# Performance work log

Measured on AMD Instinct MI355X. Metric: run time of the kernel, lower is better.

Reference implementation:

```python
import jax, jax.numpy as jnp
import numpy as np

EPS = 1e-8


def quaternion_mul(q, m):
    # Hamilton product q * m over last dim of size 4 (w, x, y, z)
    w1, x1, y1, z1 = q[..., 0], q[..., 1], q[..., 2], q[..., 3]
    w2, x2, y2, z2 = m[..., 0], m[..., 1], m[..., 2], m[..., 3]
    return jnp.stack([
        w1 * w2 - x1 * x2 - y1 * y2 - z1 * z2,
        w1 * x2 + x1 * w2 + y1 * z2 - z1 * y2,
        w1 * y2 - x1 * z2 + y1 * w2 + z1 * x2,
        w1 * z2 + x1 * y2 - y1 * x2 + z1 * w2,
    ], axis=-1)


def quaternion_normalize(q):
    n = jnp.linalg.norm(q, axis=-1, keepdims=True)
    return q / (n + EPS)


def setup_inputs() -> dict:
    key = jax.random.key(0)
    k = jax.random.split(key, 5)
    B, S, D, H = 4, 2048, 1024, 1024
    scale = 0.02
    return {
        "x": jax.random.normal(k[0], (B, S, D), dtype=jnp.float32),
        "W_in": jax.random.normal(k[1], (3 * H, D), dtype=jnp.float32) * scale,
        "b_in": jax.random.normal(k[2], (3 * H,), dtype=jnp.float32) * scale,
        "W_out": jax.random.normal(k[3], (D, 4 * H), dtype=jnp.float32) * scale,
        "b_out": jax.random.normal(k[4], (D,), dtype=jnp.float32) * scale,
    }


def reference(x, W_in, b_in, W_out, b_out):
    B, S, D = x.shape
    H = W_in.shape[0] // 3
    # input projection -> rotation parameters v in R^3 per hidden channel
    v = (jnp.einsum('bsd,ed->bse', x, W_in) + b_in).reshape(B, S, H, 3)
    # SU(2) exponential map: v -> unit quaternion
    theta = jnp.linalg.norm(v, axis=-1, keepdims=True)          # (B,S,H,1)
    axis = v / (theta + EPS)
    q_inputs = jnp.concatenate([jnp.cos(theta), jnp.sin(theta) * axis], axis=-1)  # (B,S,H,4)

    # initial identity quaternion state (B,H,4)
    m0 = jnp.zeros((B, H, 4), dtype=x.dtype).at[..., 0].set(1.0)

    def step(m, q_t):
        m_new = quaternion_normalize(quaternion_mul(q_t, m))
        return m_new, m_new

    q_seq = jnp.transpose(q_inputs, (1, 0, 2, 3))               # (S,B,H,4)
    m_final, ms = jax.lax.scan(step, m0, q_seq)                 # ms: (S,B,H,4)

    states = jnp.transpose(ms, (1, 0, 2, 3)).reshape(B, S, 4 * H)
    full_output = jnp.einsum('bsf,df->bsd', states, W_out) + b_out
    return full_output, m_final
```

## Files before the change

### kernel.cpp

```cpp
#include <hip/hip_runtime.h>
#include <hip/hip_bf16.h>
#include <stdint.h>

#define EPSF 1e-8f

typedef __attribute__((ext_vector_type(8))) short short8;
typedef __attribute__((ext_vector_type(8))) _Float16 half8;
typedef __attribute__((ext_vector_type(4))) float floatx4;

__device__ __forceinline__ unsigned short f2h(float f) {
    _Float16 h = (_Float16)f;
    return __builtin_bit_cast(unsigned short, h);
}
__device__ __forceinline__ float h2f(unsigned short u) {
    return (float)__builtin_bit_cast(_Float16, u);
}


__global__ void prep_kernel(const float4* __restrict__ x4, ushort4* __restrict__ x16,
                            const float4* __restrict__ wi4, ushort4* __restrict__ wi16,
                            const float4* __restrict__ wo4, ushort4* __restrict__ wo16,
                            int nx4, int nw4, int nwo4) {
    int i = blockIdx.x * blockDim.x + threadIdx.x;
    float4 f; ushort4 u;
    if (i < nx4) {
        f = x4[i];
        u.x = f2h(f.x); u.y = f2h(f.y); u.z = f2h(f.z); u.w = f2h(f.w);
        x16[i] = u;
    } else if (i < nx4 + nw4) {
        int j = i - nx4;
        f = wi4[j];
        u.x = f2h(f.x); u.y = f2h(f.y); u.z = f2h(f.z); u.w = f2h(f.w);
        wi16[j] = u;
    } else if (i < nx4 + nw4 + nwo4) {
        int j = i - nx4 - nw4;
        f = wo4[j];
        u.x = f2h(f.x); u.y = f2h(f.y); u.z = f2h(f.z); u.w = f2h(f.w);
        wo16[j] = u;
    }
}


__device__ __forceinline__ void gld16(const unsigned short* g, unsigned short* l) {
    __builtin_amdgcn_global_load_lds(
        (const __attribute__((address_space(1))) unsigned int*)g,
        (__attribute__((address_space(3))) unsigned int*)l, 16, 0, 0);
}

template <bool HALFOUT>
__global__ __launch_bounds__(512, 2)
void gemm8p(const unsigned short* __restrict__ Am, const unsigned short* __restrict__ Bm,
            const float* __restrict__ bias, void* __restrict__ Cv,
            int M, int N, int K) {
    constexpr int BM = 256, BN = 128, BK = 64;
    constexpr int ASZ  = BM * BK;
    constexpr int BSZ  = BN * BK;
    constexpr int SLOT = ASZ + BSZ;
    extern __shared__ unsigned short smem[];

    const int tid  = threadIdx.x;
    const int lane = tid & 63;
    const int wid  = tid >> 6;
    const int wr   = wid >> 1, wc = wid & 1;
    const int q4   = lane >> 4;
    const int m16  = lane & 15;
    const int x7   = m16 & 7;

    const int nbx = N / BN;
    const int nwg = gridDim.x;
    const int q   = nwg >> 3;
    const int wg  = blockIdx.x;
    const int sz  = (wg & 7) * q + (wg >> 3);
    const int bx  = sz % nbx, by = sz / nbx;
    const int rowA0 = by * BM, rowB0 = bx * BN;

    const int rA = tid >> 3, cA = tid & 7;
    const int cg = cA ^ (rA & 7);
    const unsigned short* srcA = Am + (size_t)(rowA0 + rA) * K + cg * 8;
    const unsigned short* srcB = Bm + (size_t)(rowB0 + rA) * K + cg * 8;
    const int dA = tid * 8;

    int aoffm[4], boffn[4];
#pragma unroll
    for (int m = 0; m < 4; ++m) aoffm[m] = (wr * 64 + m * 16 + m16) * BK;
#pragma unroll
    for (int n = 0; n < 4; ++n) boffn[n] = (wc * 64 + n * 16 + m16) * BK;

    floatx4 acc[4][4];
#pragma unroll
    for (int m = 0; m < 4; ++m)
#pragma unroll
        for (int n = 0; n < 4; ++n)
#pragma unroll
            for (int r = 0; r < 4; ++r) acc[m][n][r] = 0.f;

    const int NT = K / BK;

    auto stageA = [&](int s, int t, int j) {
        gld16(srcA + (size_t)(j * 64) * K + (size_t)t * BK,
              smem + s * SLOT + j * 4096 + dA);
    };
    auto stageB = [&](int s, int t, int j) {
        gld16(srcB + (size_t)(j * 64) * K + (size_t)t * BK,
              smem + s * SLOT + ASZ + j * 4096 + dA);
    };
    auto RD = [&](const unsigned short* tA, const unsigned short* tB, int kh,
                  short8* Ra, short8* Rb) {
        const int xo = ((kh * 4 + q4) ^ x7) * 8;
#pragma unroll
        for (int m = 0; m < 4; ++m) Ra[m] = *(const short8*)(tA + aoffm[m] + xo);
#pragma unroll
        for (int n = 0; n < 4; ++n) Rb[n] = *(const short8*)(tB + boffn[n] + xo);
    };
    auto MM = [&](short8* Ra, short8* Rb) {
        __builtin_amdgcn_s_setprio(1);
#pragma unroll
        for (int m = 0; m < 4; ++m)
#pragma unroll
            for (int n = 0; n < 4; ++n)
                acc[m][n] = __builtin_amdgcn_mfma_f32_16x16x32_f16(
                    __builtin_bit_cast(half8, Ra[m]), __builtin_bit_cast(half8, Rb[n]),
                    acc[m][n], 0, 0, 0);
        __builtin_amdgcn_s_setprio(0);
    };

#pragma unroll
    for (int j = 0; j < 4; ++j) stageA(0, 0, j);
    stageB(0, 0, 0); stageB(0, 0, 1);
#pragma unroll
    for (int j = 0; j < 4; ++j) stageA(1, 1, j);
    stageB(1, 1, 0); stageB(1, 1, 1);

    asm volatile("s_waitcnt vmcnt(6)" ::: "memory");
    __builtin_amdgcn_s_barrier();
    __builtin_amdgcn_sched_barrier(0);

    short8 RA0[4], RB0[4], RA1[4], RB1[4];
    RD(smem, smem + ASZ, 0, RA0, RB0);

    int s0 = 0;
    for (int t = 0; t < NT; ++t) {
        __builtin_amdgcn_s_barrier();
        __builtin_amdgcn_sched_barrier(0);

        int s1 = s0 + 1; if (s1 == 3) s1 = 0;
        int s2 = s1 + 1; if (s2 == 3) s2 = 0;
        const unsigned short* tA  = smem + s0 * SLOT;
        const unsigned short* tB  = tA + ASZ;
        const unsigned short* tA1 = smem + s1 * SLOT;
        const unsigned short* tB1 = tA1 + ASZ;

        if (t + 2 < NT) {
#pragma unroll
            for (int j = 0; j < 4; ++j) stageA(s2, t + 2, j);
            stageB(s2, t + 2, 0); stageB(s2, t + 2, 1);
        }

        RD(tA, tB, 1, RA1, RB1);
        MM(RA0, RB0);

        if (t + 2 < NT) asm volatile("s_waitcnt vmcnt(6)" ::: "memory");
        else            asm volatile("s_waitcnt vmcnt(0)" ::: "memory");
        __builtin_amdgcn_s_barrier();
        __builtin_amdgcn_sched_barrier(0);

        if (t + 1 < NT) RD(tA1, tB1, 0, RA0, RB0);
        MM(RA1, RB1);

        s0 = s1;
    }

#pragma unroll
    for (int m = 0; m < 4; ++m) {
#pragma unroll
        for (int n = 0; n < 4; ++n) {
            int col  = rowB0 + wc * 64 + n * 16 + m16;
            float bvl = bias[col];
#pragma unroll
            for (int r = 0; r < 4; ++r) {
                int row = rowA0 + wr * 64 + m * 16 + q4 * 4 + r;
                if (HALFOUT)
                    ((unsigned short*)Cv)[(size_t)row * N + col] = f2h(acc[m][n][r] + bvl);
                else
                    ((float*)Cv)[(size_t)row * N + col] = acc[m][n][r] + bvl;
            }
        }
    }
}


struct Q { float w, x, y, z; };

__device__ __forceinline__ Q qmul(Q a, Q b) {
    Q r;
    r.w = a.w * b.w - a.x * b.x - a.y * b.y - a.z * b.z;
    r.x = a.w * b.x + a.x * b.w + a.y * b.z - a.z * b.y;
    r.y = a.w * b.y - a.x * b.z + a.y * b.w + a.z * b.x;
    r.z = a.w * b.z + a.x * b.y - a.y * b.x + a.z * b.w;
    return r;
}
__device__ __forceinline__ Q qnorm(Q a) {
    float nn = a.w * a.w + a.x * a.x + a.y * a.y + a.z * a.z;
    float inv = __frsqrt_rn(nn);
    Q r; r.w = a.w * inv; r.x = a.x * inv; r.y = a.y * inv; r.z = a.z * inv;
    return r;
}
__device__ __forceinline__ Q vquat(float vx, float vy, float vz) {
    float th = sqrtf(vx * vx + vy * vy + vz * vz);
    float s_, c_;
    __sincosf(th, &s_, &c_);
    float k = __fdividef(s_, th + EPSF);
    Q q; q.w = c_; q.x = k * vx; q.y = k * vy; q.z = k * vz;
    return q;
}

#define SEG  32
#define NSEG 64

__global__ __launch_bounds__(256)
void seg_prod_kernel(const unsigned short* __restrict__ v, float* __restrict__ partials,
                     int S, int H) {
    const int b  = blockIdx.z;
    const int h  = blockIdx.y * 64 + (threadIdx.x & 63);
    const int sg = blockIdx.x * 4 + (threadIdx.x >> 6);
    const int s0 = sg * SEG;
    const size_t vstep = (size_t)3 * H;
    const unsigned short* vp = v + ((size_t)b * S + s0) * vstep + (size_t)h * 3;

    constexpr int CH = 8;
    float ax[CH], ay[CH], az[CH], bx[CH], by[CH], bz[CH];
#pragma unroll
    for (int i = 0; i < CH; ++i) {
        ax[i] = h2f(vp[i * vstep + 0]); ay[i] = h2f(vp[i * vstep + 1]); az[i] = h2f(vp[i * vstep + 2]);
    }
    Q c = {1.f, 0.f, 0.f, 0.f};
    const int NC = SEG / CH;
    for (int cc = 0; cc < NC; cc += 2) {
        if (cc + 1 < NC) {
            const unsigned short* p = vp + (size_t)(cc + 1) * CH * vstep;
#pragma unroll
            for (int i = 0; i < CH; ++i) {
                bx[i] = h2f(p[i * vstep + 0]); by[i] = h2f(p[i * vstep + 1]); bz[i] = h2f(p[i * vstep + 2]);
            }
        }
#pragma unroll
        for (int i = 0; i < CH; ++i) c = qmul(vquat(ax[i], ay[i], az[i]), c);
        if (cc + 2 < NC) {
            const unsigned short* p = vp + (size_t)(cc + 2) * CH * vstep;
#pragma unroll
            for (int i = 0; i < CH; ++i) {
                ax[i] = h2f(p[i * vstep + 0]); ay[i] = h2f(p[i * vstep + 1]); az[i] = h2f(p[i * vstep + 2]);
            }
        }
#pragma unroll
        for (int i = 0; i < CH; ++i) c = qmul(vquat(bx[i], by[i], bz[i]), c);
    }
    float4* dst = (float4*)(partials + (((size_t)b * NSEG + sg) * H + h) * 4);
    *dst = make_float4(c.w, c.x, c.y, c.z);
}

__global__ __launch_bounds__(256)
void apply_kernel(const unsigned short* __restrict__ v, const float* __restrict__ partials,
                  unsigned short* __restrict__ st, float* __restrict__ m_final,
                  int S, int H) {
    const int b   = blockIdx.z;
    const int hb  = blockIdx.y * 64;
    const int hl  = threadIdx.x & 63;
    const int h   = hb + hl;
    const int sg  = blockIdx.x * 4 + (threadIdx.x >> 6);
    const int s0  = sg * SEG;
    const size_t vstep = (size_t)3 * H;
    const size_t sstep = (size_t)4 * H;
    const unsigned short* vp = v + ((size_t)b * S + s0) * vstep + (size_t)h * 3;
    unsigned short* sp = st + ((size_t)b * S + s0) * sstep + (size_t)h * 4;

    const float4* pb = (const float4*)(partials) + ((size_t)b * NSEG) * H + h;
    Q R = {1.f, 0.f, 0.f, 0.f};
    int s2 = 0;
    for (; s2 + 4 <= sg; s2 += 4) {
        float4 a0 = pb[(size_t)(s2 + 0) * H];
        float4 a1 = pb[(size_t)(s2 + 1) * H];
        float4 a2 = pb[(size_t)(s2 + 2) * H];
        float4 a3 = pb[(size_t)(s2 + 3) * H];
        Q q0 = {a0.x, a0.y, a0.z, a0.w};
        Q q1 = {a1.x, a1.y, a1.z, a1.w};
        Q q2 = {a2.x, a2.y, a2.z, a2.w};
        Q q3 = {a3.x, a3.y, a3.z, a3.w};
        Q t01 = qmul(q1, q0);
        Q t23 = qmul(q3, q2);
        R = qmul(qmul(t23, t01), R);
    }
    for (; s2 < sg; ++s2) {
        float4 a = pb[(size_t)s2 * H];
        Q pq = {a.x, a.y, a.z, a.w};
        R = qmul(pq, R);
    }

    constexpr int CH = 8;
    float ax[CH], ay[CH], az[CH], bx[CH], by[CH], bz[CH];
#pragma unroll
    for (int i = 0; i < CH; ++i) {
        ax[i] = h2f(vp[i * vstep + 0]); ay[i] = h2f(vp[i * vstep + 1]); az[i] = h2f(vp[i * vstep + 2]);
    }
    const int NC = SEG / CH;
    for (int cc = 0; cc < NC; cc += 2) {
        if (cc + 1 < NC) {
            const unsigned short* pp = vp + (size_t)(cc + 1) * CH * vstep;
#pragma unroll
            for (int i = 0; i < CH; ++i) {
                bx[i] = h2f(pp[i * vstep + 0]); by[i] = h2f(pp[i * vstep + 1]); bz[i] = h2f(pp[i * vstep + 2]);
            }
        }
#pragma unroll
        for (int i = 0; i < CH; ++i) {
            R = qmul(vquat(ax[i], ay[i], az[i]), R);
            Q m = qnorm(R);
            ushort4 u; u.x = f2h(m.w); u.y = f2h(m.x); u.z = f2h(m.y); u.w = f2h(m.z);
            *(ushort4*)(sp + (size_t)(cc * CH + i) * sstep) = u;
        }
        if (cc + 2 < NC) {
            const unsigned short* pp = vp + (size_t)(cc + 2) * CH * vstep;
#pragma unroll
            for (int i = 0; i < CH; ++i) {
                ax[i] = h2f(pp[i * vstep + 0]); ay[i] = h2f(pp[i * vstep + 1]); az[i] = h2f(pp[i * vstep + 2]);
            }
        }
#pragma unroll
        for (int i = 0; i < CH; ++i) {
            R = qmul(vquat(bx[i], by[i], bz[i]), R);
            Q m = qnorm(R);
            ushort4 u; u.x = f2h(m.w); u.y = f2h(m.x); u.z = f2h(m.y); u.w = f2h(m.z);
            *(ushort4*)(sp + (size_t)((cc + 1) * CH + i) * sstep) = u;
        }
    }

    if (sg == NSEG - 1) {
        Q m = qnorm(R);
        float* mf = m_final + ((size_t)b * H + h) * 4;
        mf[0] = m.w; mf[1] = m.x; mf[2] = m.y; mf[3] = m.z;
    }
}


extern "C" void kernel_launch(void* const* d_in, const int* in_sizes, int n_in,
                              void* d_out, int out_size, void* d_ws, size_t ws_size,
                              hipStream_t stream) {
    const float* x     = (const float*)d_in[0];
    const float* W_in  = (const float*)d_in[1];
    const float* b_in  = (const float*)d_in[2];
    const float* W_out = (const float*)d_in[3];
    const float* b_out = (const float*)d_in[4];
    float* out = (float*)d_out;

    const int B = 4, S = 2048, D = 1024, H = 1024;
    const int M  = B * S;
    const int N1 = 3 * H;
    const int K1 = D;
    const int N2 = D;
    const int K2 = 4 * H;

    char* ws = (char*)d_ws;
    unsigned short* v    = (unsigned short*)(ws);
    unsigned short* st   = (unsigned short*)(ws + 50331648u);
    unsigned short* x16  = (unsigned short*)(ws + 50331648u);
    unsigned short* wi16 = (unsigned short*)(ws + 50331648u + 16777216u);
    unsigned short* wo16 = (unsigned short*)(ws + 117440512u);

    float* partials = out;

    const int nx  = M * K1;
    const int nw  = N1 * K1;
    const int nwo = N2 * K2;
    const int n4  = (nx + nw + nwo) / 4;

    constexpr int LDSB = 147456;
    static int attr_done = 0;
    if (!attr_done) {
        hipFuncSetAttribute(reinterpret_cast<const void*>(&gemm8p<true>),
                            hipFuncAttributeMaxDynamicSharedMemorySize, LDSB);
        hipFuncSetAttribute(reinterpret_cast<const void*>(&gemm8p<false>),
                            hipFuncAttributeMaxDynamicSharedMemorySize, LDSB);
        attr_done = 1;
    }

    prep_kernel<<<(n4 + 255) / 256, 256, 0, stream>>>(
        (const float4*)x, (ushort4*)x16, (const float4*)W_in, (ushort4*)wi16,
        (const float4*)W_out, (ushort4*)wo16, nx / 4, nw / 4, nwo / 4);

    gemm8p<true><<<dim3((M / 256) * (N1 / 128)), 512, LDSB, stream>>>(
        x16, wi16, b_in, v, M, N1, K1);

    dim3 sg_grid(NSEG / 4, H / 64, B);
    seg_prod_kernel<<<sg_grid, 256, 0, stream>>>(v, partials, S, H);
    apply_kernel<<<sg_grid, 256, 0, stream>>>(v, partials, st, out + (size_t)M * D, S, H);

    gemm8p<false><<<dim3((M / 256) * (N2 / 128)), 512, LDSB, stream>>>(
        st, wo16, b_out, out, M, N2, K2);
}
```

Before: 310.8 us.

## Switch GEMMs to 256x256 tiles with split-K atomics for output projection

Replaces the 256x128 GEMM with a 256x256-tile kernel that uses a new swizzled LDS layout and a 4-slot half-tile pipeline, giving more MFMA work per loaded byte. The output projection is split over K into two parts, with results accumulated by float atomicAdd into a zeroed output buffer, so more workgroups run on the small grid. The cost is an extra memset, atomic traffic in the epilogue, higher register pressure from 32 accumulator tiles, and sum-order nondeterminism.

```diff
diff --git a/kernel.cpp b/kernel.cpp
--- a/kernel.cpp
+++ b/kernel.cpp
@@ -40,149 +40,133 @@
     }
 }
 
-
 __device__ __forceinline__ void gld16(const unsigned short* g, unsigned short* l) {
     __builtin_amdgcn_global_load_lds(
         (const __attribute__((address_space(1))) unsigned int*)g,
         (__attribute__((address_space(3))) unsigned int*)l, 16, 0, 0);
 }
 
+
 template <bool HALFOUT>
 __global__ __launch_bounds__(512, 2)
-void gemm8p(const unsigned short* __restrict__ Am, const unsigned short* __restrict__ Bm,
-            const float* __restrict__ bias, void* __restrict__ Cv,
-            int M, int N, int K) {
-    constexpr int BM = 256, BN = 128, BK = 64;
-    constexpr int ASZ  = BM * BK;
-    constexpr int BSZ  = BN * BK;
-    constexpr int SLOT = ASZ + BSZ;
+void gemm256k(const unsigned short* __restrict__ Am, const unsigned short* __restrict__ Bm,
+              const float* __restrict__ bias, void* __restrict__ Cv,
+              int M, int N, int K, int nsplit) {
     extern __shared__ unsigned short smem[];
 
     const int tid  = threadIdx.x;
     const int lane = tid & 63;
     const int wid  = tid >> 6;
-    const int wr   = wid >> 1, wc = wid & 1;
+    const int wr   = wid >> 2;
+    const int wc   = wid & 3;
     const int q4   = lane >> 4;
     const int m16  = lane & 15;
-    const int x7   = m16 & 7;
-
-    const int nbx = N / BN;
+
+    const int nbx = N >> 8;
     const int nwg = gridDim.x;
-    const int q   = nwg >> 3;
-    const int wg  = blockIdx.x;
-    const int sz  = (wg & 7) * q + (wg >> 3);
-    const int bx  = sz % nbx, by = sz / nbx;
-    const int rowA0 = by * BM, rowB0 = bx * BN;
-
-    const int rA = tid >> 3, cA = tid & 7;
-    const int cg = cA ^ (rA & 7);
-    const unsigned short* srcA = Am + (size_t)(rowA0 + rA) * K + cg * 8;
-    const unsigned short* srcB = Bm + (size_t)(rowB0 + rA) * K + cg * 8;
-    const int dA = tid * 8;
-
-    int aoffm[4], boffn[4];
-#pragma unroll
-    for (int m = 0; m < 4; ++m) aoffm[m] = (wr * 64 + m * 16 + m16) * BK;
-#pragma unroll
-    for (int n = 0; n < 4; ++n) boffn[n] = (wc * 64 + n * 16 + m16) * BK;
-
-    floatx4 acc[4][4];
-#pragma unroll
-    for (int m = 0; m < 4; ++m)
+    const int qq  = nwg >> 3;
+    const int sz  = (blockIdx.x & 7) * qq + (blockIdx.x >> 3);
+    const int per = nwg / nsplit;
+    const int ks  = sz / per;
+    const int rm  = sz % per;
+    const int by  = rm / nbx, bx = rm % nbx;
+    const int rowA0 = by * 256, rowB0 = bx * 256;
+    const int Kper = K / nsplit;
+    const int k0   = ks * Kper;
+
+    int g_i[2], g_c[2];
+#pragma unroll
+    for (int j = 0; j < 2; ++j) {
+        int L  = tid * 8 + j * 4096;
+        int lr = L >> 6;
+        int x  = ((L >> 3) & 7) ^ (lr & 7);
+        g_i[j] = lr * 2 + (x >> 2);
+        g_c[j] = x & 3;
+    }
+
+    int aoff[8], boff[4];
+#pragma unroll
+    for (int f = 0; f < 8; ++f) {
+        int i = wr * 128 + f * 16 + m16;
+        aoff[f] = (i >> 1) * 64 + (((((i & 1) << 2) | q4) ^ ((i >> 1) & 7)) * 8);
+    }
+#pragma unroll
+    for (int f = 0; f < 4; ++f) {
+        int i = wc * 64 + f * 16 + m16;
+        boff[f] = 8192 + (i >> 1) * 64 + (((((i & 1) << 2) | q4) ^ ((i >> 1) & 7)) * 8);
+    }
+
+    floatx4 acc[8][4];
+#pragma unroll
+    for (int m = 0; m < 8; ++m)
 #pragma unroll
         for (int n = 0; n < 4; ++n)
 #pragma unroll
             for (int r = 0; r < 4; ++r) acc[m][n][r] = 0.f;
 
-    const int NT = K / BK;
-
-    auto stageA = [&](int s, int t, int j) {
-        gld16(srcA + (size_t)(j * 64) * K + (size_t)t * BK,
-              smem + s * SLOT + j * 4096 + dA);
+    auto STG = [&](int s) {
+        const int rb = (s & 3) * 16384;
+        const int tb = k0 + (s >> 1) * 64 + (s & 1) * 32;
+#pragma unroll
+        for (int j = 0; j < 2; ++j)
+            gld16(Am + (size_t)(rowA0 + g_i[j]) * K + tb + g_c[j] * 8,
+                  smem + rb + j * 4096 + tid * 8);
+#pragma unroll
+        for (int j = 0; j < 2; ++j)
+            gld16(Bm + (size_t)(rowB0 + g_i[j]) * K + tb + g_c[j] * 8,
+                  smem + rb + 8192 + j * 4096 + tid * 8);
     };
-    auto stageB = [&](int s, int t, int j) {
-        gld16(srcB + (size_t)(j * 64) * K + (size_t)t * BK,
-              smem + s * SLOT + ASZ + j * 4096 + dA);
-    };
-    auto RD = [&](const unsigned short* tA, const unsigned short* tB, int kh,
-                  short8* Ra, short8* Rb) {
-        const int xo = ((kh * 4 + q4) ^ x7) * 8;
-#pragma unroll
-        for (int m = 0; m < 4; ++m) Ra[m] = *(const short8*)(tA + aoffm[m] + xo);
-#pragma unroll
-        for (int n = 0; n < 4; ++n) Rb[n] = *(const short8*)(tB + boffn[n] + xo);
-    };
-    auto MM = [&](short8* Ra, short8* Rb) {
+
+    auto HALF = [&](int s) {
+        const unsigned short* rb = smem + (s & 3) * 16384;
+        short8 Af[8], Bf[4];
+#pragma unroll
+        for (int f = 0; f < 4; ++f) Bf[f] = *(const short8*)(rb + boff[f]);
+#pragma unroll
+        for (int f = 0; f < 8; ++f) Af[f] = *(const short8*)(rb + aoff[f]);
         __builtin_amdgcn_s_setprio(1);
 #pragma unroll
-        for (int m = 0; m < 4; ++m)
-#pragma unroll
-            for (int n = 0; n < 4; ++n)
-                acc[m][n] = __builtin_amdgcn_mfma_f32_16x16x32_f16(
-                    __builtin_bit_cast(half8, Ra[m]), __builtin_bit_cast(half8, Rb[n]),
-                    acc[m][n], 0, 0, 0);
+        for (int mf = 0; mf < 8; ++mf)
+#pragma unroll
+            for (int nf = 0; nf < 4; ++nf)
+                acc[mf][nf] = __builtin_amdgcn_mfma_f32_16x16x32_f16(
+                    __builtin_bit_cast(half8, Af[mf]), __builtin_bit_cast(half8, Bf[nf]),
+                    acc[mf][nf], 0, 0, 0);
         __builtin_amdgcn_s_setprio(0);
     };
 
-#pragma unroll
-    for (int j = 0; j < 4; ++j) stageA(0, 0, j);
-    stageB(0, 0, 0); stageB(0, 0, 1);
-#pragma unroll
-    for (int j = 0; j < 4; ++j) stageA(1, 1, j);
-    stageB(1, 1, 0); stageB(1, 1, 1);
-
-    asm volatile("s_waitcnt vmcnt(6)" ::: "memory");
-    __builtin_amdgcn_s_barrier();
-    __builtin_amdgcn_sched_barrier(0);
-
-    short8 RA0[4], RB0[4], RA1[4], RB1[4];
-    RD(smem, smem + ASZ, 0, RA0, RB0);
-
-    int s0 = 0;
+    const int NT = Kper / 64;
+
+    STG(0); STG(1);
+
     for (int t = 0; t < NT; ++t) {
+        asm volatile("s_waitcnt vmcnt(4)" ::: "memory");
         __builtin_amdgcn_s_barrier();
         __builtin_amdgcn_sched_barrier(0);
-
-        int s1 = s0 + 1; if (s1 == 3) s1 = 0;
-        int s2 = s1 + 1; if (s2 == 3) s2 = 0;
-        const unsigned short* tA  = smem + s0 * SLOT;
-        const unsigned short* tB  = tA + ASZ;
-        const unsigned short* tA1 = smem + s1 * SLOT;
-        const unsigned short* tB1 = tA1 + ASZ;
-
-        if (t + 2 < NT) {
-#pragma unroll
-            for (int j = 0; j < 4; ++j) stageA(s2, t + 2, j);
-            stageB(s2, t + 2, 0); stageB(s2, t + 2, 1);
-        }
-
-        RD(tA, tB, 1, RA1, RB1);
-        MM(RA0, RB0);
-
-        if (t + 2 < NT) asm volatile("s_waitcnt vmcnt(6)" ::: "memory");
+        if (t + 1 < NT) STG(2 * t + 2);
+        HALF(2 * t);
+
+        if (t + 1 < NT) asm volatile("s_waitcnt vmcnt(4)" ::: "memory");
         else            asm volatile("s_waitcnt vmcnt(0)" ::: "memory");
         __builtin_amdgcn_s_barrier();
         __builtin_amdgcn_sched_barrier(0);
-
-        if (t + 1 < NT) RD(tA1, tB1, 0, RA0, RB0);
-        MM(RA1, RB1);
-
-        s0 = s1;
-    }
-
-#pragma unroll
-    for (int m = 0; m < 4; ++m) {
-#pragma unroll
-        for (int n = 0; n < 4; ++n) {
-            int col  = rowB0 + wc * 64 + n * 16 + m16;
-            float bvl = bias[col];
+        if (t + 1 < NT) STG(2 * t + 3);
+        HALF(2 * t + 1);
+    }
+
+#pragma unroll
+    for (int mf = 0; mf < 8; ++mf) {
+#pragma unroll
+        for (int nf = 0; nf < 4; ++nf) {
+            int col  = rowB0 + wc * 64 + nf * 16 + m16;
+            float bvl = (ks == 0) ? bias[col] : 0.f;
 #pragma unroll
             for (int r = 0; r < 4; ++r) {
-                int row = rowA0 + wr * 64 + m * 16 + q4 * 4 + r;
+                int row = rowA0 + wr * 128 + mf * 16 + q4 * 4 + r;
                 if (HALFOUT)
-                    ((unsigned short*)Cv)[(size_t)row * N + col] = f2h(acc[m][n][r] + bvl);
+                    ((unsigned short*)Cv)[(size_t)row * N + col] = f2h(acc[mf][nf][r] + bvl);
                 else
-                    ((float*)Cv)[(size_t)row * N + col] = acc[m][n][r] + bvl;
+                    atomicAdd(&((float*)Cv)[(size_t)row * N + col], acc[mf][nf][r] + bvl);
             }
         }
     }
@@ -373,12 +357,12 @@
     const int nwo = N2 * K2;
     const int n4  = (nx + nw + nwo) / 4;
 
-    constexpr int LDSB = 147456;
+    constexpr int LDSB = 131072;
     static int attr_done = 0;
     if (!attr_done) {
-        hipFuncSetAttribute(reinterpret_cast<const void*>(&gemm8p<true>),
+        hipFuncSetAttribute(reinterpret_cast<const void*>(&gemm256k<true>),
                             hipFuncAttributeMaxDynamicSharedMemorySize, LDSB);
-        hipFuncSetAttribute(reinterpret_cast<const void*>(&gemm8p<false>),
+        hipFuncSetAttribute(reinterpret_cast<const void*>(&gemm256k<false>),
                             hipFuncAttributeMaxDynamicSharedMemorySize, LDSB);
         attr_done = 1;
     }
@@ -387,13 +371,14 @@
         (const float4*)x, (ushort4*)x16, (const float4*)W_in, (ushort4*)wi16,
         (const float4*)W_out, (ushort4*)wo16, nx / 4, nw / 4, nwo / 4);
 
-    gemm8p<true><<<dim3((M / 256) * (N1 / 128)), 512, LDSB, stream>>>(
-        x16, wi16, b_in, v, M, N1, K1);
+    gemm256k<true><<<dim3((M / 256) * (N1 / 256)), 512, LDSB, stream>>>(
+        x16, wi16, b_in, v, M, N1, K1, 1);
 
     dim3 sg_grid(NSEG / 4, H / 64, B);
     seg_prod_kernel<<<sg_grid, 256, 0, stream>>>(v, partials, S, H);
     apply_kernel<<<sg_grid, 256, 0, stream>>>(v, partials, st, out + (size_t)M * D, S, H);
 
-    gemm8p<false><<<dim3((M / 256) * (N2 / 128)), 512, LDSB, stream>>>(
-        st, wo16, b_out, out, M, N2, K2);
-}
+    hipMemsetAsync(out, 0, (size_t)M * D * sizeof(float), stream);
+    gemm256k<false><<<dim3((M / 256) * (N2 / 256) * 2), 512, LDSB, stream>>>(
+        st, wo16, b_out, out, M, N2, K2, 2);
+}
```

New measurement: 340.3 us. 1.09x slower.
